# Performance work log

Measured on AMD Instinct MI355X. Metric: run time of the kernel, lower is better.

The kernel has to match this reference:

```python
import jax, jax.numpy as jnp
import numpy as np

# irreps config: (multiplicity, l) for "128x0e + 64x1o + 32x2e" (in == out)
IRREPS = [(128, 0), (64, 1), (32, 2)]


def setup_inputs() -> dict:
    key = jax.random.key(0)
    k0, k1, k2, k3 = jax.random.split(key, 4)
    N = 200000
    dim = sum(mul * (2 * l + 1) for mul, l in IRREPS)  # 480
    x = jax.random.normal(k0, (N, dim), dtype=jnp.float32)
    W0 = jax.random.normal(k1, (128, 128), dtype=jnp.float32)
    W1 = jax.random.normal(k2, (64, 64), dtype=jnp.float32)
    W2 = jax.random.normal(k3, (32, 32), dtype=jnp.float32)
    return {"x": x, "W0": W0, "W1": W1, "W2": W2}


def _irrep_linear(x, weights):
    # x: [N, dim_in]; per-irrep: reshape block to [N, mul, 2l+1], contract mul dim,
    # scale by 1/sqrt(fan_in) = 1/sqrt(mul_in) (e3nn default path normalization).
    outs = []
    off = 0
    for (mul, l), W in zip(IRREPS, weights):
        d = 2 * l + 1
        blk = x[:, off:off + mul * d].reshape(-1, mul, d)  # [N, mul, d]
        alpha = 1.0 / np.sqrt(mul)
        y = jnp.einsum('nid,io->nod', blk, W) * jnp.float32(alpha)  # [N, mul_out, d]
        outs.append(y.reshape(-1, mul * d))
        off += mul * d
    return jnp.concatenate(outs, axis=-1)  # [N, dim_out]


def reference(x, W0, W1, W2):
    return _irrep_linear(x, (W0, W1, W2))
```

## Files before the change

### kernel.cpp

```cpp
#include <hip/hip_runtime.h>

typedef _Float16 v8h __attribute__((ext_vector_type(8)));
typedef float    v4f __attribute__((ext_vector_type(4)));

#define MFMA16(a, b, c) __builtin_amdgcn_mfma_f32_16x16x32_f16((a), (b), (c), 0, 0, 0)

#define GLL16(gptr, lptr)                                                        \
  __builtin_amdgcn_global_load_lds((const __attribute__((address_space(1))) void*)(gptr), \
                                   (__attribute__((address_space(3))) void*)(lptr), 16, 0, 0)


__global__ void build_frags_k(const float* __restrict__ W0, const float* __restrict__ W1,
                              const float* __restrict__ W2, v8h* __restrict__ frag) {
  const int f = blockIdx.x;
  const int lane = threadIdx.x;
  int ot, kt;
  if (f < 32)       { ot = f >> 2;           kt = f & 3; }
  else if (f < 104) { int q = f - 32;  ot = 8 + q / 6;  kt = 4 + q % 6; }
  else              { int q = f - 104; ot = 20 + q / 5; kt = 10 + q % 5; }
  const int n  = ot * 16 + (lane & 15);
  const int kb = kt * 32 + (lane >> 4) * 8;
  v8h v;
#pragma unroll
  for (int e = 0; e < 8; ++e) {
    const int k = kb + e;
    float wv = 0.0f;
    if (k < 128) {
      if (n < 128) wv = W0[k * 128 + n] * 0.08838834764831845f;
    } else if (k < 320) {
      if (n >= 128 && n < 320) {
        const int i = k - 128, o = n - 128;
        if (i % 3 == o % 3) wv = W1[(i / 3) * 64 + (o / 3)] * 0.125f;
      }
    } else {
      if (n >= 320) {
        const int i = k - 320, o = n - 320;
        if (i % 5 == o % 5) wv = W2[(i / 5) * 32 + (o / 5)] * 0.17677669529663687f;
      }
    }
    v[e] = (_Float16)wv;
  }
  frag[f * 64 + lane] = v;
}

template <int V>
__device__ __forceinline__ void wave_main(const float* __restrict__ x,
                                          const v8h* __restrict__ frag,
                                          float* __restrict__ out,
                                          unsigned char* sm, int t, int t0, int t1) {
  const int lane = t & 63;
  const int w    = t >> 6;
  const int r16  = lane & 15;
  const int g    = lane >> 4;

  constexpr int G = (V == 0) ? 8 : 7;
  constexpr int S = (V == 2) ? 6 : 8;

  constexpr int NF = (V == 0) ? 21 : (V == 1) ? 20 : 15;
  v8h f[NF];
  {
    const int fb0 = w * 4;
    const int fb1 = 32 + w * 6;
#pragma unroll
    for (int k = 0; k < 4; ++k) f[k] = frag[(fb0 + k) * 64 + lane];
#pragma unroll
    for (int k = 0; k < 6; ++k) f[4 + k] = frag[(fb1 + k) * 64 + lane];
    if constexpr (V == 0) {
      const int fb2 = 32 + (8 + w) * 6;
      const int fb3 = 104 + (4 + w) * 5;
#pragma unroll
      for (int k = 0; k < 6; ++k) f[10 + k] = frag[(fb2 + k) * 64 + lane];
#pragma unroll
      for (int k = 0; k < 5; ++k) f[16 + k] = frag[(fb3 + k) * 64 + lane];
    } else if constexpr (V == 1) {
      const int fb2 = 104 + (w - 4) * 5;
      const int fb3 = 104 + (w + 4) * 5;
#pragma unroll
      for (int k = 0; k < 5; ++k) f[10 + k] = frag[(fb2 + k) * 64 + lane];
#pragma unroll
      for (int k = 0; k < 5; ++k) f[15 + k] = frag[(fb3 + k) * 64 + lane];
    } else {
      const int fb2 = 104 + (w - 4) * 5;
#pragma unroll
      for (int k = 0; k < 5; ++k) f[10 + k] = frag[(fb2 + k) * 64 + lane];
    }
  }

  auto stage = [&](int tt, int bsel) {
    const unsigned char* xt = (const unsigned char*)x + (size_t)tt * 61440u;
    unsigned char* buf = sm + bsel * 61440;
#pragma unroll
    for (int i = 0; i < 8; ++i) {
      if (i < 7 || t < 256) {
        const unsigned gl = (unsigned)(i * 512 + t);
        const unsigned r  = gl / 120u;
        const unsigned j  = gl - r * 120u;
        GLL16(xt + r * 1920u + ((j ^ (r & 7u)) << 4), buf + i * 8192 + w * 1024);
      }
    }
  };

#define LDAF(kt, dst)                                                                       \
  {                                                                                         \
    const unsigned j0 = (unsigned)((kt) * 8 + g * 2);                                       \
    const float4 lo = *reinterpret_cast<const float4*>(smc + rb + (((j0) ^ q) << 4));       \
    const float4 hi = *reinterpret_cast<const float4*>(smc + rb + ((((j0) + 1) ^ q) << 4)); \
    v8h v_;                                                                                 \
    v_[0] = (_Float16)lo.x; v_[1] = (_Float16)lo.y;                                         \
    v_[2] = (_Float16)lo.z; v_[3] = (_Float16)lo.w;                                         \
    v_[4] = (_Float16)hi.x; v_[5] = (_Float16)hi.y;                                         \
    v_[6] = (_Float16)hi.z; v_[7] = (_Float16)hi.w;                                         \
    dst = v_;                                                                               \
  }

  auto compute = [&](int tt, int bsel) {
    const unsigned char* smc = sm + bsel * 61440;
#pragma unroll
    for (int sl = 0; sl < 2; ++sl) {
      const unsigned row = (unsigned)(sl * 16 + r16);
      const unsigned rb  = row * 1920u;
      const unsigned q   = row & 7u;
      float* const ob = out + ((size_t)tt * 32 + sl * 16 + r16) * 480 + g * 4;
      {
        v8h x0[4];
#pragma unroll
        for (int k = 0; k < 4; ++k) LDAF(k, x0[k]);
        v4f a0 = {0.f, 0.f, 0.f, 0.f};
#pragma unroll
        for (int k = 0; k < 4; ++k) a0 = MFMA16(f[k], x0[k], a0);
        *reinterpret_cast<v4f*>(ob + w * 16) = a0;
      }
      {
        v8h x1[6];
#pragma unroll
        for (int k = 0; k < 6; ++k) LDAF(4 + k, x1[k]);
        v4f a1 = {0.f, 0.f, 0.f, 0.f};
#pragma unroll
        for (int k = 0; k < 6; ++k) a1 = MFMA16(f[4 + k], x1[k], a1);
        *reinterpret_cast<v4f*>(ob + (8 + w) * 16) = a1;
        if constexpr (V == 0) {
          v4f a2 = {0.f, 0.f, 0.f, 0.f};
#pragma unroll
          for (int k = 0; k < 6; ++k) a2 = MFMA16(f[10 + k], x1[k], a2);
          *reinterpret_cast<v4f*>(ob + (16 + w) * 16) = a2;
        }
      }
      {
        v8h x2[5];
#pragma unroll
        for (int k = 0; k < 5; ++k) LDAF(10 + k, x2[k]);
        if constexpr (V == 0) {
          v4f a3 = {0.f, 0.f, 0.f, 0.f};
#pragma unroll
          for (int k = 0; k < 5; ++k) a3 = MFMA16(f[16 + k], x2[k], a3);
          *reinterpret_cast<v4f*>(ob + (24 + w) * 16) = a3;
        } else if constexpr (V == 1) {
          v4f a2 = {0.f, 0.f, 0.f, 0.f}, a3 = {0.f, 0.f, 0.f, 0.f};
#pragma unroll
          for (int k = 0; k < 5; ++k) {
            a2 = MFMA16(f[10 + k], x2[k], a2);
            a3 = MFMA16(f[15 + k], x2[k], a3);
          }
          *reinterpret_cast<v4f*>(ob + (16 + w) * 16) = a2;
          *reinterpret_cast<v4f*>(ob + (24 + w) * 16) = a3;
        } else {
          v4f a2 = {0.f, 0.f, 0.f, 0.f};
#pragma unroll
          for (int k = 0; k < 5; ++k) a2 = MFMA16(f[10 + k], x2[k], a2);
          *reinterpret_cast<v4f*>(ob + (16 + w) * 16) = a2;
        }
      }
    }
  };

  stage(t0, 0);
  stage(t0 + 1, 1);
  asm volatile("s_waitcnt vmcnt(%0)" :: "n"(G) : "memory");
  __builtin_amdgcn_s_barrier();
  compute(t0, 0);
  __builtin_amdgcn_s_barrier();

  int tt = t0 + 1;
  for (; tt < t1 - 1; ++tt) {
    const int cur = (tt - t0) & 1;
    stage(tt + 1, cur ^ 1);
    asm volatile("s_waitcnt vmcnt(%0)" :: "n"(G + S) : "memory");
    __builtin_amdgcn_s_barrier();
    compute(tt, cur);
    __builtin_amdgcn_s_barrier();
  }
  {
    const int cur = (tt - t0) & 1;
    asm volatile("s_waitcnt vmcnt(%0)" :: "n"(S) : "memory");
    __builtin_amdgcn_s_barrier();
    compute(tt, cur);
  }
#undef LDAF
}

__global__ __launch_bounds__(512, 2) void irrep_linear_k(
    const float* __restrict__ x, const v8h* __restrict__ frag, float* __restrict__ out,
    int base_tpb, int rem) {
  __shared__ __align__(16) unsigned char sm[2 * 61440];
  const int t = threadIdx.x;
  const int b = blockIdx.x;
  const int t0 = b * base_tpb + (b < rem ? b : rem);
  const int t1 = t0 + base_tpb + (b < rem ? 1 : 0);
  const int w = t >> 6;
  if (w < 4)      wave_main<0>(x, frag, out, sm, t, t0, t1);
  else if (w < 6) wave_main<1>(x, frag, out, sm, t, t0, t1);
  else            wave_main<2>(x, frag, out, sm, t, t0, t1);
}

extern "C" void kernel_launch(void* const* d_in, const int* in_sizes, int n_in,
                              void* d_out, int out_size, void* d_ws, size_t ws_size,
                              hipStream_t stream) {
  const float* x  = (const float*)d_in[0];
  const float* W0 = (const float*)d_in[1];
  const float* W1 = (const float*)d_in[2];
  const float* W2 = (const float*)d_in[3];
  float* out = (float*)d_out;
  v8h* frag = (v8h*)d_ws;

  build_frags_k<<<154, 64, 0, stream>>>(W0, W1, W2, frag);

  const int N = in_sizes[0] / 480;
  const int n_tiles = N / 32;
  const int nblk = 256;
  const int base_tpb = n_tiles / nblk;
  const int rem = n_tiles - base_tpb * nblk;
  irrep_linear_k<<<nblk, 512, 0, stream>>>(x, frag, out, base_tpb, rem);
}
```

Measured before the change: 175.1 us.

## Specialize waves per irrep block so each loads only its own input slice

Reassigns output tiles so each wave handles a single irrep block: waves 0-1 do l=0, waves 2-5 do l=1, waves 6-7 do l=2. Each wave now reads only the LDS k-range its block needs, instead of reading several ranges and doing multiple MFMA chains. This cuts LDS reads and f32-to-f16 conversions per wave. It also rebalances MFMA counts across waves. The waitcnt constants are now template parameters, and launch bounds drop from 2 to 1 blocks per CU, which allows up to 25 weight fragments to stay in registers.

```diff
diff --git a/kernel.cpp b/kernel.cpp
--- a/kernel.cpp
+++ b/kernel.cpp
@@ -43,7 +43,7 @@
   frag[f * 64 + lane] = v;
 }
 
-template <int V>
+template <int V, int G>
 __device__ __forceinline__ void wave_main(const float* __restrict__ x,
                                           const v8h* __restrict__ frag,
                                           float* __restrict__ out,
@@ -53,37 +53,28 @@
   const int r16  = lane & 15;
   const int g    = lane >> 4;
 
-  constexpr int G = (V == 0) ? 8 : 7;
-  constexpr int S = (V == 2) ? 6 : 8;
-
-  constexpr int NF = (V == 0) ? 21 : (V == 1) ? 20 : 15;
+  constexpr int S  = (V == 0) ? 8 : (V == 1) ? 6 : 10;
+  constexpr int NF = (V == 0) ? 16 : (V == 1) ? 18 : 25;
+
   v8h f[NF];
-  {
-    const int fb0 = w * 4;
-    const int fb1 = 32 + w * 6;
-#pragma unroll
-    for (int k = 0; k < 4; ++k) f[k] = frag[(fb0 + k) * 64 + lane];
-#pragma unroll
-    for (int k = 0; k < 6; ++k) f[4 + k] = frag[(fb1 + k) * 64 + lane];
-    if constexpr (V == 0) {
-      const int fb2 = 32 + (8 + w) * 6;
-      const int fb3 = 104 + (4 + w) * 5;
-#pragma unroll
-      for (int k = 0; k < 6; ++k) f[10 + k] = frag[(fb2 + k) * 64 + lane];
-#pragma unroll
-      for (int k = 0; k < 5; ++k) f[16 + k] = frag[(fb3 + k) * 64 + lane];
-    } else if constexpr (V == 1) {
-      const int fb2 = 104 + (w - 4) * 5;
-      const int fb3 = 104 + (w + 4) * 5;
-#pragma unroll
-      for (int k = 0; k < 5; ++k) f[10 + k] = frag[(fb2 + k) * 64 + lane];
-#pragma unroll
-      for (int k = 0; k < 5; ++k) f[15 + k] = frag[(fb3 + k) * 64 + lane];
-    } else {
-      const int fb2 = 104 + (w - 4) * 5;
-#pragma unroll
-      for (int k = 0; k < 5; ++k) f[10 + k] = frag[(fb2 + k) * 64 + lane];
-    }
+  if constexpr (V == 0) {
+#pragma unroll
+    for (int i = 0; i < 4; ++i)
+#pragma unroll
+      for (int k = 0; k < 4; ++k)
+        f[i * 4 + k] = frag[((w + 2 * i) * 4 + k) * 64 + lane];
+  } else if constexpr (V == 1) {
+#pragma unroll
+    for (int i = 0; i < 3; ++i)
+#pragma unroll
+      for (int k = 0; k < 6; ++k)
+        f[i * 6 + k] = frag[(32 + (w - 2 + 4 * i) * 6 + k) * 64 + lane];
+  } else {
+#pragma unroll
+    for (int i = 0; i < 5; ++i)
+#pragma unroll
+      for (int k = 0; k < 5; ++k)
+        f[i * 5 + k] = frag[(104 + (w - 6 + 2 * i) * 5 + k) * 64 + lane];
   }
 
   auto stage = [&](int tt, int bsel) {
@@ -121,53 +112,38 @@
       const unsigned rb  = row * 1920u;
       const unsigned q   = row & 7u;
       float* const ob = out + ((size_t)tt * 32 + sl * 16 + r16) * 480 + g * 4;
-      {
-        v8h x0[4];
-#pragma unroll
-        for (int k = 0; k < 4; ++k) LDAF(k, x0[k]);
-        v4f a0 = {0.f, 0.f, 0.f, 0.f};
-#pragma unroll
-        for (int k = 0; k < 4; ++k) a0 = MFMA16(f[k], x0[k], a0);
-        *reinterpret_cast<v4f*>(ob + w * 16) = a0;
-      }
-      {
-        v8h x1[6];
-#pragma unroll
-        for (int k = 0; k < 6; ++k) LDAF(4 + k, x1[k]);
-        v4f a1 = {0.f, 0.f, 0.f, 0.f};
-#pragma unroll
-        for (int k = 0; k < 6; ++k) a1 = MFMA16(f[4 + k], x1[k], a1);
-        *reinterpret_cast<v4f*>(ob + (8 + w) * 16) = a1;
-        if constexpr (V == 0) {
-          v4f a2 = {0.f, 0.f, 0.f, 0.f};
-#pragma unroll
-          for (int k = 0; k < 6; ++k) a2 = MFMA16(f[10 + k], x1[k], a2);
-          *reinterpret_cast<v4f*>(ob + (16 + w) * 16) = a2;
+      if constexpr (V == 0) {
+        v8h xr[4];
+#pragma unroll
+        for (int k = 0; k < 4; ++k) LDAF(k, xr[k]);
+#pragma unroll
+        for (int i = 0; i < 4; ++i) {
+          v4f a = {0.f, 0.f, 0.f, 0.f};
+#pragma unroll
+          for (int k = 0; k < 4; ++k) a = MFMA16(f[i * 4 + k], xr[k], a);
+          *reinterpret_cast<v4f*>(ob + (w + 2 * i) * 16) = a;
         }
-      }
-      {
-        v8h x2[5];
-#pragma unroll
-        for (int k = 0; k < 5; ++k) LDAF(10 + k, x2[k]);
-        if constexpr (V == 0) {
-          v4f a3 = {0.f, 0.f, 0.f, 0.f};
-#pragma unroll
-          for (int k = 0; k < 5; ++k) a3 = MFMA16(f[16 + k], x2[k], a3);
-          *reinterpret_cast<v4f*>(ob + (24 + w) * 16) = a3;
-        } else if constexpr (V == 1) {
-          v4f a2 = {0.f, 0.f, 0.f, 0.f}, a3 = {0.f, 0.f, 0.f, 0.f};
-#pragma unroll
-          for (int k = 0; k < 5; ++k) {
-            a2 = MFMA16(f[10 + k], x2[k], a2);
-            a3 = MFMA16(f[15 + k], x2[k], a3);
-          }
-          *reinterpret_cast<v4f*>(ob + (16 + w) * 16) = a2;
-          *reinterpret_cast<v4f*>(ob + (24 + w) * 16) = a3;
-        } else {
-          v4f a2 = {0.f, 0.f, 0.f, 0.f};
-#pragma unroll
-          for (int k = 0; k < 5; ++k) a2 = MFMA16(f[10 + k], x2[k], a2);
-          *reinterpret_cast<v4f*>(ob + (16 + w) * 16) = a2;
+      } else if constexpr (V == 1) {
+        v8h xr[6];
+#pragma unroll
+        for (int k = 0; k < 6; ++k) LDAF(4 + k, xr[k]);
+#pragma unroll
+        for (int i = 0; i < 3; ++i) {
+          v4f a = {0.f, 0.f, 0.f, 0.f};
+#pragma unroll
+          for (int k = 0; k < 6; ++k) a = MFMA16(f[i * 6 + k], xr[k], a);
+          *reinterpret_cast<v4f*>(ob + (6 + w + 4 * i) * 16) = a;
+        }
+      } else {
+        v8h xr[5];
+#pragma unroll
+        for (int k = 0; k < 5; ++k) LDAF(10 + k, xr[k]);
+#pragma unroll
+        for (int i = 0; i < 5; ++i) {
+          v4f a = {0.f, 0.f, 0.f, 0.f};
+#pragma unroll
+          for (int k = 0; k < 5; ++k) a = MFMA16(f[i * 5 + k], xr[k], a);
+          *reinterpret_cast<v4f*>(ob + (14 + w + 2 * i) * 16) = a;
         }
       }
     }
@@ -198,7 +174,7 @@
 #undef LDAF
 }
 
-__global__ __launch_bounds__(512, 2) void irrep_linear_k(
+__global__ __launch_bounds__(512, 1) void irrep_linear_k(
     const float* __restrict__ x, const v8h* __restrict__ frag, float* __restrict__ out,
     int base_tpb, int rem) {
   __shared__ __align__(16) unsigned char sm[2 * 61440];
@@ -207,9 +183,10 @@
   const int t0 = b * base_tpb + (b < rem ? b : rem);
   const int t1 = t0 + base_tpb + (b < rem ? 1 : 0);
   const int w = t >> 6;
-  if (w < 4)      wave_main<0>(x, frag, out, sm, t, t0, t1);
-  else if (w < 6) wave_main<1>(x, frag, out, sm, t, t0, t1);
-  else            wave_main<2>(x, frag, out, sm, t, t0, t1);
+  if (w < 2)      wave_main<0, 8>(x, frag, out, sm, t, t0, t1);
+  else if (w < 4) wave_main<1, 8>(x, frag, out, sm, t, t0, t1);
+  else if (w < 6) wave_main<1, 7>(x, frag, out, sm, t, t0, t1);
+  else            wave_main<2, 7>(x, frag, out, sm, t, t0, t1);
 }
 
 extern "C" void kernel_launch(void* const* d_in, const int* in_sizes, int n_in,
```

Result: no change. 172.8 us (-1.3%).
